# Kernel tuning notes

Measured on AMD Instinct MI355X. Metric: run time of the kernel, lower is better.

The kernel has to match this reference:

```python
import jax, jax.numpy as jnp
import numpy as np

# --- Clifford algebra constants for a 4D Euclidean space (MULTIVECTOR_DIM = 16) ---
# grades 0..4 have dims (1,4,6,4,1); component index -> grade:
GRADE_OF = np.array([0] + [1]*4 + [2]*6 + [3]*4 + [4], dtype=np.int64)  # [16]
# reversion sign per grade k: (-1)^{k(k-1)/2}
_REV_PER_GRADE = np.array([1.0, 1.0, -1.0, -1.0, 1.0], dtype=np.float32)
REVERSION = jnp.asarray(_REV_PER_GRADE[GRADE_OF])            # [16]
# scalar part of geometric product of orthonormal basis blades: diag of reversion signs
SCALAR_TABLE = jnp.asarray(np.diag(_REV_PER_GRADE[GRADE_OF]).astype(np.float32))  # [16,16]
SCALE = 1.0 / np.sqrt(16.0)

B, S, H, M = 4, 2048, 8, 16


def _block_masks():
    block = (GRADE_OF[:, None] == GRADE_OF[None, :]).astype(np.float32)  # [16,16]
    bias = ((GRADE_OF == 0) | (GRADE_OF == 4)).astype(np.float32)        # [16]
    return jnp.asarray(block), jnp.asarray(bias)


def setup_inputs() -> dict:
    key = jax.random.key(0)
    ks = jax.random.split(key, 10)
    block, bias = _block_masks()
    def w_in(k):   # [16, H, 16], zero outside grade blocks (j -> i within same grade)
        return jax.random.normal(k, (M, H, M), jnp.float32) * 0.1 * block[:, None, :]
    def b_in(k):   # [H, 16], only grade-0 / grade-4 components have bias
        return jax.random.normal(k, (H, M), jnp.float32) * 0.1 * bias[None, :]
    x = jax.random.normal(ks[0], (B, S, M), jnp.float32)
    return {
        "x": x,
        "wq": w_in(ks[1]), "bq": b_in(ks[2]),
        "wk": w_in(ks[3]), "bk": b_in(ks[4]),
        "wv": w_in(ks[5]), "bv": b_in(ks[6]),
        "wo": jax.random.normal(ks[7], (H, M, M), jnp.float32) * 0.1 * block[None, :, :],
        "bo": jax.random.normal(ks[8], (M,), jnp.float32) * 0.1 * bias,
    }


def reference(x, wq, bq, wk, bk, wv, bv, wo, bo):
    # per-grade Q/K/V projections, packed as block-sparse linears over 16 components
    q = jnp.einsum('bsj,jhi->bhsi', x, wq) + bq[None, :, None, :]  # [B,H,S,16]
    k = jnp.einsum('bsj,jhi->bhsi', x, wk) + bk[None, :, None, :]
    v = jnp.einsum('bsj,jhi->bhsi', x, wv) + bv[None, :, None, :]
    k_rev = k * REVERSION[None, None, None, :]
    # scalar part of geometric product <Q * reverse(K)>_0 via fixed bilinear table
    scores = jnp.einsum('bhqi,bhkj,ij->bhqk', q, k_rev, SCALAR_TABLE) * SCALE
    attn = jax.nn.softmax(scores, axis=-1)                         # [B,H,S,S]
    head = jnp.einsum('bhqk,bhki->bhqi', attn, v)                  # [B,H,S,16]
    # per-grade output projections (block over heads x grade components)
    out = jnp.einsum('bhqj,hji->bqi', head, wo) + bo               # [B,S,16]
    return out
```

## Files before the change

### kernel.cpp

```cpp
#include <hip/hip_runtime.h>

#define BB 4
#define SS 2048
#define HH 8
#define MM 16

#define QSCALE 0.36067376022224085f

typedef __attribute__((ext_vector_type(8)))  short short8;
typedef __attribute__((ext_vector_type(4)))  int   int4v;
typedef __attribute__((ext_vector_type(4)))  float f32x4;
typedef __attribute__((ext_vector_type(16))) float f32x16;

static constexpr size_t NQKV = (size_t)BB * HH * SS * MM;

__device__ __forceinline__ int pk_bf16(float lo, float hi) {
    int r;
    asm("v_cvt_pk_bf16_f32 %0, %1, %2" : "=v"(r) : "v"(lo), "v"(hi));
    return r;
}

__device__ __forceinline__ void proj16(const float xr[16], const float* __restrict__ w,
                                       const float* __restrict__ bias, int h, float out[16]) {
#pragma unroll
    for (int i = 0; i < 16; i++) out[i] = bias[(h << 4) + i];
#pragma unroll
    for (int j = 0; j < 16; j++) {
        float xj = xr[j];
        const float* wr = w + (((j * HH) + h) << 4);
#pragma unroll
        for (int i = 0; i < 16; i++) out[i] = fmaf(xj, wr[i], out[i]);
    }
}

__device__ __forceinline__ void pack_store(ushort* dst, const float o[16], float scale) {
    int4v w0, w1;
#pragma unroll
    for (int j = 0; j < 4; j++) w0[j] = pk_bf16(o[2*j] * scale,     o[2*j+1] * scale);
#pragma unroll
    for (int j = 0; j < 4; j++) w1[j] = pk_bf16(o[8+2*j] * scale,   o[8+2*j+1] * scale);
    int4v* p = (int4v*)dst;
    p[0] = w0; p[1] = w1;
}

__global__ __launch_bounds__(256) void proj_kernel(
    const float* __restrict__ x,
    const float* __restrict__ wq, const float* __restrict__ bq,
    const float* __restrict__ wk, const float* __restrict__ bk,
    const float* __restrict__ wv, const float* __restrict__ bv,
    ushort* __restrict__ qb, ushort* __restrict__ kb, ushort* __restrict__ vb)
{
    int h  = blockIdx.x >> 5;
    int bs = ((blockIdx.x & 31) << 8) + threadIdx.x;
    int b  = bs >> 11;

    float xr[16];
    const float4* x4 = (const float4*)(x + (size_t)bs * MM);
#pragma unroll
    for (int j = 0; j < 4; j++) {
        float4 t = x4[j];
        xr[j*4+0] = t.x; xr[j*4+1] = t.y; xr[j*4+2] = t.z; xr[j*4+3] = t.w;
    }

    size_t orow = (((size_t)(b * HH + h) * SS) + (bs & 2047)) * MM;
    float o[16];

    proj16(xr, wq, bq, h, o);  pack_store(qb + orow, o, QSCALE);
    proj16(xr, wk, bk, h, o);  pack_store(kb + orow, o, 1.0f);
    proj16(xr, wv, bv, h, o);  pack_store(vb + orow, o, 1.0f);
}

__global__ __launch_bounds__(256, 8) void attn_kernel(
    const ushort* __restrict__ qb, const ushort* __restrict__ kb,
    const ushort* __restrict__ vb, float* __restrict__ hb)
{
    __shared__ ushort Vl[4][32 * 72];

    int tid = threadIdx.x;
    int w = tid >> 6;
    int lane = tid & 63;
    int n = lane & 31, c = lane >> 5;

    int nb = ((blockIdx.x & 7) << 8) | (blockIdx.x >> 3);
    int bh = nb >> 6, qt = nb & 63;
    size_t base = (size_t)bh * SS * MM;
    const ushort* Qg = qb + base;
    const ushort* Kg = kb + base;
    const ushort* Vg = vb + base;

    int q = qt * 32 + n;
    short8 qf = *(const short8*)(Qg + (size_t)q * MM + c * 8);

    ushort* Vt = Vl[w];
    for (int i = lane; i < 72; i += 64) {
        Vt[16 * 72 + i] = 0x3F80;
        Vt[20 * 72 + i] = 0x3F80;
    }

    f32x16 oacc = 0;
    const f32x16 zacc = 0;

    int k0 = w * 512;
    int4v vwa = *(const int4v*)(Vg + (size_t)(k0 + lane) * MM);
    int4v vwb = *(const int4v*)(Vg + (size_t)(k0 + lane) * MM + 8);

    for (int t = 0; t < 8; t++) {
        union { int4v v; ushort s[8]; } ua, ub;
        ua.v = vwa; ub.v = vwb;
#pragma unroll
        for (int j = 0; j < 8; j++) Vt[j * 72 + lane] = ua.s[j];
#pragma unroll
        for (int j = 0; j < 8; j++) Vt[(8 + j) * 72 + lane] = ub.s[j];
        if (t != 7) {
            vwa = *(const int4v*)(Vg + (size_t)(k0 + (t + 1) * 64 + lane) * MM);
            vwb = *(const int4v*)(Vg + (size_t)(k0 + (t + 1) * 64 + lane) * MM + 8);
        }

#pragma unroll
        for (int sub = 0; sub < 2; sub++) {
            short8 kf = *(const short8*)(Kg + (size_t)(k0 + t * 64 + sub * 32 + n) * MM + c * 8);
            f32x16 s = __builtin_amdgcn_mfma_f32_32x32x16_bf16(kf, qf, zacc, 0, 0, 0);

            float pv[16];
#pragma unroll
            for (int r = 0; r < 16; r++) pv[r] = __builtin_amdgcn_exp2f(s[r]);

            int a0 = pk_bf16(pv[0],  pv[1]);
            int a1 = pk_bf16(pv[2],  pv[3]);
            int a2 = pk_bf16(pv[4],  pv[5]);
            int a3 = pk_bf16(pv[6],  pv[7]);
            int a4 = pk_bf16(pv[8],  pv[9]);
            int a5 = pk_bf16(pv[10], pv[11]);
            int a6 = pk_bf16(pv[12], pv[13]);
            int a7 = pk_bf16(pv[14], pv[15]);

            int w0 = a0, w2 = a2;
            asm("v_permlane32_swap_b32 %0, %1" : "+v"(w0), "+v"(w2));
            int w1 = a1, w3 = a3;
            asm("v_permlane32_swap_b32 %0, %1" : "+v"(w1), "+v"(w3));
            int u0 = a4, u2 = a6;
            asm("v_permlane32_swap_b32 %0, %1" : "+v"(u0), "+v"(u2));
            int u1 = a5, u3 = a7;
            asm("v_permlane32_swap_b32 %0, %1" : "+v"(u1), "+v"(u3));

            int4v bi1 = {w0, w1, w2, w3};
            int4v bi2 = {u0, u1, u2, u3};
            short8 B1 = __builtin_bit_cast(short8, bi1);
            short8 B2 = __builtin_bit_cast(short8, bi2);

            int vr = lane & 31;
            short8 vf1 = *(const short8*)&Vt[vr * 72 + sub * 32 + c * 8];
            short8 vf2 = *(const short8*)&Vt[vr * 72 + sub * 32 + 16 + c * 8];
            oacc = __builtin_amdgcn_mfma_f32_32x32x16_bf16(vf1, B1, oacc, 0, 0, 0);
            oacc = __builtin_amdgcn_mfma_f32_32x32x16_bf16(vf2, B2, oacc, 0, 0, 0);
        }
    }

    __syncthreads();
    float* mg = (float*)&Vl[0][0];
    if (w != 0) {
        float* dst = mg + (size_t)(w - 1) * 576 + n * 18;
#pragma unroll
        for (int j = 0; j < 4; j++) dst[4 * c + j]     = oacc[j];
#pragma unroll
        for (int j = 0; j < 4; j++) dst[8 + 4 * c + j] = oacc[4 + j];
        dst[16 + c] = oacc[8];
    }
    __syncthreads();
    if (w == 0) {
        float l = oacc[8];
        float o0[4], o1[4];
#pragma unroll
        for (int j = 0; j < 4; j++) { o0[j] = oacc[j]; o1[j] = oacc[4 + j]; }
#pragma unroll
        for (int p = 0; p < 3; p++) {
            const float* src = mg + (size_t)p * 576 + n * 18;
#pragma unroll
            for (int j = 0; j < 4; j++) o0[j] += src[4 * c + j];
#pragma unroll
            for (int j = 0; j < 4; j++) o1[j] += src[8 + 4 * c + j];
            l += src[16 + c];
        }
        float inv = 1.0f / l;
        float* orow = hb + base + (size_t)q * MM;
        f32x4 v0 = {o0[0] * inv, o0[1] * inv, o0[2] * inv, o0[3] * inv};
        f32x4 v1 = {o1[0] * inv, o1[1] * inv, o1[2] * inv, o1[3] * inv};
        *(f32x4*)(orow + 4 * c) = v0;
        *(f32x4*)(orow + 8 + 4 * c) = v1;
    }
}

__global__ __launch_bounds__(128) void outproj_kernel(
    const float* __restrict__ hb, const float* __restrict__ wo,
    const float* __restrict__ bo, float* __restrict__ out)
{
    int tid = threadIdx.x;
    int row = blockIdx.x * 64 + (tid >> 1);
    int hh = tid & 1;
    int b = row >> 11, s = row & 2047;

    float acc[16];
#pragma unroll
    for (int i = 0; i < 16; i++) acc[i] = 0.0f;

    for (int hi = 0; hi < 4; hi++) {
        int h = hh * 4 + hi;
        const float* hr = hb + ((size_t)(b * 8 + h) * SS + s) * MM;
        float hv[16];
        const f32x4* h4 = (const f32x4*)hr;
#pragma unroll
        for (int j = 0; j < 4; j++) {
            f32x4 tv = h4[j];
            hv[j*4+0] = tv[0]; hv[j*4+1] = tv[1]; hv[j*4+2] = tv[2]; hv[j*4+3] = tv[3];
        }
#pragma unroll
        for (int j = 0; j < 16; j++) {
            float hj = hv[j];
            const float* wr = wo + (((h << 4) + j) << 4);
#pragma unroll
            for (int i = 0; i < 16; i++) acc[i] = fmaf(hj, wr[i], acc[i]);
        }
    }

#pragma unroll
    for (int i = 0; i < 16; i++) acc[i] += __shfl_xor(acc[i], 1);

    if (hh == 0) {
        float* op = out + (size_t)row * MM;
#pragma unroll
        for (int j = 0; j < 4; j++) {
            f32x4 v = {acc[4*j+0] + bo[4*j+0], acc[4*j+1] + bo[4*j+1],
                       acc[4*j+2] + bo[4*j+2], acc[4*j+3] + bo[4*j+3]};
            *(f32x4*)(op + 4*j) = v;
        }
    }
}

extern "C" void kernel_launch(void* const* d_in, const int* in_sizes, int n_in,
                              void* d_out, int out_size, void* d_ws, size_t ws_size,
                              hipStream_t stream) {
    const float* x  = (const float*)d_in[0];
    const float* wq = (const float*)d_in[1];
    const float* bq = (const float*)d_in[2];
    const float* wk = (const float*)d_in[3];
    const float* bk = (const float*)d_in[4];
    const float* wv = (const float*)d_in[5];
    const float* bv = (const float*)d_in[6];
    const float* wo = (const float*)d_in[7];
    const float* bo = (const float*)d_in[8];
    float* out = (float*)d_out;

    ushort* qb = (ushort*)d_ws;
    ushort* kb = qb + NQKV;
    ushort* vb = kb + NQKV;
    float*  hb = (float*)(vb + NQKV);

    proj_kernel<<<256, 256, 0, stream>>>(x, wq, bq, wk, bk, wv, bv, qb, kb, vb);
    attn_kernel<<<2048, 256, 0, stream>>>(qb, kb, vb, hb);
    outproj_kernel<<<128, 128, 0, stream>>>(hb, wo, bo, out);
}
```

Measured before the change: 44.68 us.

## Store V transposed in global, drop LDS staging, add exp-minus-one precision split

The projection kernel now writes V transposed (dimension-major, sequence contiguous). This lets the attention kernel load V fragments straight from global memory instead of staging them through per-wave LDS, which removes the LDS writes and reads. The attention probabilities are packed as exp2(s)-1 in bf16 to keep more precision. The missing constant part is restored with extra MFMAs against a ones operand, so the PV MFMA count doubles. The unroll structure and launch bounds also change, and the V store in the projection becomes scattered 2-byte writes.

```diff
diff --git a/kernel.cpp b/kernel.cpp
--- a/kernel.cpp
+++ b/kernel.cpp
@@ -48,11 +48,13 @@
     const float* __restrict__ wq, const float* __restrict__ bq,
     const float* __restrict__ wk, const float* __restrict__ bk,
     const float* __restrict__ wv, const float* __restrict__ bv,
-    ushort* __restrict__ qb, ushort* __restrict__ kb, ushort* __restrict__ vb)
+    ushort* __restrict__ qb, ushort* __restrict__ kb, ushort* __restrict__ vt)
 {
     int h  = blockIdx.x >> 5;
     int bs = ((blockIdx.x & 31) << 8) + threadIdx.x;
     int b  = bs >> 11;
+    int s  = bs & 2047;
+    int bh = b * HH + h;
 
     float xr[16];
     const float4* x4 = (const float4*)(x + (size_t)bs * MM);
@@ -62,19 +64,25 @@
         xr[j*4+0] = t.x; xr[j*4+1] = t.y; xr[j*4+2] = t.z; xr[j*4+3] = t.w;
     }
 
-    size_t orow = (((size_t)(b * HH + h) * SS) + (bs & 2047)) * MM;
+    size_t orow = ((size_t)bh * SS + s) * MM;
     float o[16];
 
     proj16(xr, wq, bq, h, o);  pack_store(qb + orow, o, QSCALE);
     proj16(xr, wk, bk, h, o);  pack_store(kb + orow, o, 1.0f);
-    proj16(xr, wv, bv, h, o);  pack_store(vb + orow, o, 1.0f);
-}
-
-__global__ __launch_bounds__(256, 8) void attn_kernel(
+
+    proj16(xr, wv, bv, h, o);
+    ushort* vrow = vt + (size_t)bh * 16 * SS + s;
+#pragma unroll
+    for (int d = 0; d < 16; d++) {
+        vrow[(size_t)d * SS] = (ushort)pk_bf16(o[d], o[d]);
+    }
+}
+
+__global__ __launch_bounds__(256) void attn_kernel(
     const ushort* __restrict__ qb, const ushort* __restrict__ kb,
-    const ushort* __restrict__ vb, float* __restrict__ hb)
+    const ushort* __restrict__ vt, float* __restrict__ hb)
 {
-    __shared__ ushort Vl[4][32 * 72];
+    __shared__ float mg[3 * 32 * 18];
 
     int tid = threadIdx.x;
     int w = tid >> 6;
@@ -86,78 +94,70 @@
     size_t base = (size_t)bh * SS * MM;
     const ushort* Qg = qb + base;
     const ushort* Kg = kb + base;
-    const ushort* Vg = vb + base;
+    const ushort* Vtg = vt + (size_t)bh * 16 * SS;
 
     int q = qt * 32 + n;
     short8 qf = *(const short8*)(Qg + (size_t)q * MM + c * 8);
 
-    ushort* Vt = Vl[w];
-    for (int i = lane; i < 72; i += 64) {
-        Vt[16 * 72 + i] = 0x3F80;
-        Vt[20 * 72 + i] = 0x3F80;
-    }
+    short8 vfill = 0;
+    if (n == 16 || n == 20) {
+#pragma unroll
+        for (int j = 0; j < 8; j++) vfill[j] = (short)0x3F80;
+    }
+    short8 onesb;
+#pragma unroll
+    for (int j = 0; j < 8; j++) onesb[j] = (short)0x3F80;
 
     f32x16 oacc = 0;
     const f32x16 zacc = 0;
 
     int k0 = w * 512;
-    int4v vwa = *(const int4v*)(Vg + (size_t)(k0 + lane) * MM);
-    int4v vwb = *(const int4v*)(Vg + (size_t)(k0 + lane) * MM + 8);
-
-    for (int t = 0; t < 8; t++) {
-        union { int4v v; ushort s[8]; } ua, ub;
-        ua.v = vwa; ub.v = vwb;
-#pragma unroll
-        for (int j = 0; j < 8; j++) Vt[j * 72 + lane] = ua.s[j];
-#pragma unroll
-        for (int j = 0; j < 8; j++) Vt[(8 + j) * 72 + lane] = ub.s[j];
-        if (t != 7) {
-            vwa = *(const int4v*)(Vg + (size_t)(k0 + (t + 1) * 64 + lane) * MM);
-            vwb = *(const int4v*)(Vg + (size_t)(k0 + (t + 1) * 64 + lane) * MM + 8);
-        }
-
-#pragma unroll
-        for (int sub = 0; sub < 2; sub++) {
-            short8 kf = *(const short8*)(Kg + (size_t)(k0 + t * 64 + sub * 32 + n) * MM + c * 8);
-            f32x16 s = __builtin_amdgcn_mfma_f32_32x32x16_bf16(kf, qf, zacc, 0, 0, 0);
-
-            float pv[16];
-#pragma unroll
-            for (int r = 0; r < 16; r++) pv[r] = __builtin_amdgcn_exp2f(s[r]);
-
-            int a0 = pk_bf16(pv[0],  pv[1]);
-            int a1 = pk_bf16(pv[2],  pv[3]);
-            int a2 = pk_bf16(pv[4],  pv[5]);
-            int a3 = pk_bf16(pv[6],  pv[7]);
-            int a4 = pk_bf16(pv[8],  pv[9]);
-            int a5 = pk_bf16(pv[10], pv[11]);
-            int a6 = pk_bf16(pv[12], pv[13]);
-            int a7 = pk_bf16(pv[14], pv[15]);
-
-            int w0 = a0, w2 = a2;
-            asm("v_permlane32_swap_b32 %0, %1" : "+v"(w0), "+v"(w2));
-            int w1 = a1, w3 = a3;
-            asm("v_permlane32_swap_b32 %0, %1" : "+v"(w1), "+v"(w3));
-            int u0 = a4, u2 = a6;
-            asm("v_permlane32_swap_b32 %0, %1" : "+v"(u0), "+v"(u2));
-            int u1 = a5, u3 = a7;
-            asm("v_permlane32_swap_b32 %0, %1" : "+v"(u1), "+v"(u3));
-
-            int4v bi1 = {w0, w1, w2, w3};
-            int4v bi2 = {u0, u1, u2, u3};
-            short8 B1 = __builtin_bit_cast(short8, bi1);
-            short8 B2 = __builtin_bit_cast(short8, bi2);
-
-            int vr = lane & 31;
-            short8 vf1 = *(const short8*)&Vt[vr * 72 + sub * 32 + c * 8];
-            short8 vf2 = *(const short8*)&Vt[vr * 72 + sub * 32 + 16 + c * 8];
-            oacc = __builtin_amdgcn_mfma_f32_32x32x16_bf16(vf1, B1, oacc, 0, 0, 0);
-            oacc = __builtin_amdgcn_mfma_f32_32x32x16_bf16(vf2, B2, oacc, 0, 0, 0);
-        }
-    }
-
-    __syncthreads();
-    float* mg = (float*)&Vl[0][0];
+    const ushort* Kp  = Kg + (size_t)(k0 + n) * MM + c * 8;
+    const ushort* Vp  = Vtg + (size_t)n * SS + k0 + c * 8;
+
+#pragma unroll 2
+    for (int sub = 0; sub < 16; sub++) {
+        short8 kf = *(const short8*)(Kp + sub * 32 * MM);
+        f32x16 s = __builtin_amdgcn_mfma_f32_32x32x16_bf16(kf, qf, zacc, 0, 0, 0);
+
+        float pv[16];
+#pragma unroll
+        for (int r = 0; r < 16; r++) pv[r] = __builtin_amdgcn_exp2f(s[r]);
+#pragma unroll
+        for (int r = 0; r < 16; r++) pv[r] = pv[r] - 1.0f;
+
+        int a0 = pk_bf16(pv[0],  pv[1]);
+        int a1 = pk_bf16(pv[2],  pv[3]);
+        int a2 = pk_bf16(pv[4],  pv[5]);
+        int a3 = pk_bf16(pv[6],  pv[7]);
+        int a4 = pk_bf16(pv[8],  pv[9]);
+        int a5 = pk_bf16(pv[10], pv[11]);
+        int a6 = pk_bf16(pv[12], pv[13]);
+        int a7 = pk_bf16(pv[14], pv[15]);
+
+        int w0 = a0, w2 = a2;
+        asm("v_permlane32_swap_b32 %0, %1" : "+v"(w0), "+v"(w2));
+        int w1 = a1, w3 = a3;
+        asm("v_permlane32_swap_b32 %0, %1" : "+v"(w1), "+v"(w3));
+        int u0 = a4, u2 = a6;
+        asm("v_permlane32_swap_b32 %0, %1" : "+v"(u0), "+v"(u2));
+        int u1 = a5, u3 = a7;
+        asm("v_permlane32_swap_b32 %0, %1" : "+v"(u1), "+v"(u3));
+
+        int4v bi1 = {w0, w1, w2, w3};
+        int4v bi2 = {u0, u1, u2, u3};
+        short8 B1 = __builtin_bit_cast(short8, bi1);
+        short8 B2 = __builtin_bit_cast(short8, bi2);
+
+        const ushort* vsub = Vp + sub * 32;
+        short8 vf1 = (n < 16) ? *(const short8*)(vsub)      : vfill;
+        short8 vf2 = (n < 16) ? *(const short8*)(vsub + 16) : vfill;
+        oacc = __builtin_amdgcn_mfma_f32_32x32x16_bf16(vf1, onesb, oacc, 0, 0, 0);
+        oacc = __builtin_amdgcn_mfma_f32_32x32x16_bf16(vf1, B1,    oacc, 0, 0, 0);
+        oacc = __builtin_amdgcn_mfma_f32_32x32x16_bf16(vf2, onesb, oacc, 0, 0, 0);
+        oacc = __builtin_amdgcn_mfma_f32_32x32x16_bf16(vf2, B2,    oacc, 0, 0, 0);
+    }
+
     if (w != 0) {
         float* dst = mg + (size_t)(w - 1) * 576 + n * 18;
 #pragma unroll
@@ -252,10 +252,10 @@
 
     ushort* qb = (ushort*)d_ws;
     ushort* kb = qb + NQKV;
-    ushort* vb = kb + NQKV;
-    float*  hb = (float*)(vb + NQKV);
-
-    proj_kernel<<<256, 256, 0, stream>>>(x, wq, bq, wk, bk, wv, bv, qb, kb, vb);
-    attn_kernel<<<2048, 256, 0, stream>>>(qb, kb, vb, hb);
+    ushort* vt = kb + NQKV;
+    float*  hb = (float*)(vt + NQKV);
+
+    proj_kernel<<<256, 256, 0, stream>>>(x, wq, bq, wk, bk, wv, bv, qb, kb, vt);
+    attn_kernel<<<2048, 256, 0, stream>>>(qb, kb, vt, hb);
     outproj_kernel<<<128, 128, 0, stream>>>(hb, wo, bo, out);
 }
```

Measured after the change: 55.22 us. +23.6%, slower.

## Share staged K/V tiles across two query waves and center exp to improve bf16 precision

Applied to the files above, without the earlier changes.

Blocks now hold 512 threads, and each 128-thread group serves 64 queries with two waves that share K and V tiles staged in LDS. K now comes from shared memory instead of per-wave global loads, which halves global K/V traffic per query. Probabilities are computed as exp2(s)-1 before bf16 packing, and the missing term is restored with column sums of V and a constant 2048 added to the normalizer. This adds two block barriers per tile and a per-tile column-sum pass.

```diff
diff --git a/kernel.cpp b/kernel.cpp
--- a/kernel.cpp
+++ b/kernel.cpp
@@ -70,117 +70,170 @@
     proj16(xr, wv, bv, h, o);  pack_store(vb + orow, o, 1.0f);
 }
 
-__global__ __launch_bounds__(256, 8) void attn_kernel(
+__global__ __launch_bounds__(512) void attn_kernel(
     const ushort* __restrict__ qb, const ushort* __restrict__ kb,
     const ushort* __restrict__ vb, float* __restrict__ hb)
 {
-    __shared__ ushort Vl[4][32 * 72];
+    __shared__ ushort stage[4][3840];
 
     int tid = threadIdx.x;
-    int w = tid >> 6;
+    int grp = tid >> 7, t7 = tid & 127;
+    int wid2 = (tid >> 6) & 1;
     int lane = tid & 63;
     int n = lane & 31, c = lane >> 5;
 
-    int nb = ((blockIdx.x & 7) << 8) | (blockIdx.x >> 3);
-    int bh = nb >> 6, qt = nb & 63;
+    int nb = ((blockIdx.x & 7) << 7) | (blockIdx.x >> 3);
+    int bh = nb >> 5, qt = nb & 31;
     size_t base = (size_t)bh * SS * MM;
     const ushort* Qg = qb + base;
     const ushort* Kg = kb + base;
     const ushort* Vg = vb + base;
 
-    int q = qt * 32 + n;
+    int q = qt * 64 + wid2 * 32 + n;
     short8 qf = *(const short8*)(Qg + (size_t)q * MM + c * 8);
 
-    ushort* Vt = Vl[w];
-    for (int i = lane; i < 72; i += 64) {
+    ushort* Kl = &stage[grp][0];
+    ushort* Vt = &stage[grp][1536];
+
+    for (int i = t7; i < 72; i += 128) {
         Vt[16 * 72 + i] = 0x3F80;
         Vt[20 * 72 + i] = 0x3F80;
-    }
+#pragma unroll
+        for (int r = 17; r < 20; r++) Vt[r * 72 + i] = 0;
+#pragma unroll
+        for (int r = 21; r < 32; r++) Vt[r * 72 + i] = 0;
+    }
+
+    int k0 = grp * 512;
+    int srow = t7 >> 1, shalf = t7 & 1;
+
+    {
+        int4v kw = *(const int4v*)(Kg + (size_t)(k0 + srow) * MM + shalf * 8);
+        int4v vw = *(const int4v*)(Vg + (size_t)(k0 + srow) * MM + shalf * 8);
+        *(int4v*)&Kl[srow * 24 + shalf * 8] = kw;
+        union { int4v v; ushort s[8]; } vu; vu.v = vw;
+#pragma unroll
+        for (int j = 0; j < 8; j++) Vt[(8 * shalf + j) * 72 + srow] = vu.s[j];
+    }
+    __syncthreads();
 
     f32x16 oacc = 0;
     const f32x16 zacc = 0;
-
-    int k0 = w * 512;
-    int4v vwa = *(const int4v*)(Vg + (size_t)(k0 + lane) * MM);
-    int4v vwb = *(const int4v*)(Vg + (size_t)(k0 + lane) * MM + 8);
+    float cs = 0.0f;
+    int csd = lane >> 2, cspart = lane & 3;
 
     for (int t = 0; t < 8; t++) {
-        union { int4v v; ushort s[8]; } ua, ub;
-        ua.v = vwa; ub.v = vwb;
-#pragma unroll
-        for (int j = 0; j < 8; j++) Vt[j * 72 + lane] = ua.s[j];
-#pragma unroll
-        for (int j = 0; j < 8; j++) Vt[(8 + j) * 72 + lane] = ub.s[j];
+        int4v kw2, vw2;
         if (t != 7) {
-            vwa = *(const int4v*)(Vg + (size_t)(k0 + (t + 1) * 64 + lane) * MM);
-            vwb = *(const int4v*)(Vg + (size_t)(k0 + (t + 1) * 64 + lane) * MM + 8);
+            kw2 = *(const int4v*)(Kg + (size_t)(k0 + (t + 1) * 64 + srow) * MM + shalf * 8);
+            vw2 = *(const int4v*)(Vg + (size_t)(k0 + (t + 1) * 64 + srow) * MM + shalf * 8);
         }
 
 #pragma unroll
         for (int sub = 0; sub < 2; sub++) {
-            short8 kf = *(const short8*)(Kg + (size_t)(k0 + t * 64 + sub * 32 + n) * MM + c * 8);
+            short8 kf = *(const short8*)&Kl[(sub * 32 + n) * 24 + c * 8];
+            short8 vf1 = *(const short8*)&Vt[n * 72 + sub * 32 + c * 8];
+            short8 vf2 = *(const short8*)&Vt[n * 72 + sub * 32 + 16 + c * 8];
             f32x16 s = __builtin_amdgcn_mfma_f32_32x32x16_bf16(kf, qf, zacc, 0, 0, 0);
 
-            float pv[16];
-#pragma unroll
-            for (int r = 0; r < 16; r++) pv[r] = __builtin_amdgcn_exp2f(s[r]);
-
-            int a0 = pk_bf16(pv[0],  pv[1]);
-            int a1 = pk_bf16(pv[2],  pv[3]);
-            int a2 = pk_bf16(pv[4],  pv[5]);
-            int a3 = pk_bf16(pv[6],  pv[7]);
-            int a4 = pk_bf16(pv[8],  pv[9]);
-            int a5 = pk_bf16(pv[10], pv[11]);
-            int a6 = pk_bf16(pv[12], pv[13]);
-            int a7 = pk_bf16(pv[14], pv[15]);
-
+            float p0 = __builtin_amdgcn_exp2f(s[0])  - 1.0f;
+            float p1 = __builtin_amdgcn_exp2f(s[1])  - 1.0f;
+            float p2 = __builtin_amdgcn_exp2f(s[2])  - 1.0f;
+            float p3 = __builtin_amdgcn_exp2f(s[3])  - 1.0f;
+            float p4 = __builtin_amdgcn_exp2f(s[4])  - 1.0f;
+            float p5 = __builtin_amdgcn_exp2f(s[5])  - 1.0f;
+            float p6 = __builtin_amdgcn_exp2f(s[6])  - 1.0f;
+            float p7 = __builtin_amdgcn_exp2f(s[7])  - 1.0f;
+            int a0 = pk_bf16(p0, p1), a1 = pk_bf16(p2, p3);
+            int a2 = pk_bf16(p4, p5), a3 = pk_bf16(p6, p7);
             int w0 = a0, w2 = a2;
             asm("v_permlane32_swap_b32 %0, %1" : "+v"(w0), "+v"(w2));
             int w1 = a1, w3 = a3;
             asm("v_permlane32_swap_b32 %0, %1" : "+v"(w1), "+v"(w3));
+            int4v bi1 = {w0, w1, w2, w3};
+            short8 B1 = __builtin_bit_cast(short8, bi1);
+            oacc = __builtin_amdgcn_mfma_f32_32x32x16_bf16(vf1, B1, oacc, 0, 0, 0);
+
+            float p8  = __builtin_amdgcn_exp2f(s[8])  - 1.0f;
+            float p9  = __builtin_amdgcn_exp2f(s[9])  - 1.0f;
+            float p10 = __builtin_amdgcn_exp2f(s[10]) - 1.0f;
+            float p11 = __builtin_amdgcn_exp2f(s[11]) - 1.0f;
+            float p12 = __builtin_amdgcn_exp2f(s[12]) - 1.0f;
+            float p13 = __builtin_amdgcn_exp2f(s[13]) - 1.0f;
+            float p14 = __builtin_amdgcn_exp2f(s[14]) - 1.0f;
+            float p15 = __builtin_amdgcn_exp2f(s[15]) - 1.0f;
+            int a4 = pk_bf16(p8,  p9),  a5 = pk_bf16(p10, p11);
+            int a6 = pk_bf16(p12, p13), a7 = pk_bf16(p14, p15);
             int u0 = a4, u2 = a6;
             asm("v_permlane32_swap_b32 %0, %1" : "+v"(u0), "+v"(u2));
             int u1 = a5, u3 = a7;
             asm("v_permlane32_swap_b32 %0, %1" : "+v"(u1), "+v"(u3));
-
-            int4v bi1 = {w0, w1, w2, w3};
             int4v bi2 = {u0, u1, u2, u3};
-            short8 B1 = __builtin_bit_cast(short8, bi1);
             short8 B2 = __builtin_bit_cast(short8, bi2);
-
-            int vr = lane & 31;
-            short8 vf1 = *(const short8*)&Vt[vr * 72 + sub * 32 + c * 8];
-            short8 vf2 = *(const short8*)&Vt[vr * 72 + sub * 32 + 16 + c * 8];
-            oacc = __builtin_amdgcn_mfma_f32_32x32x16_bf16(vf1, B1, oacc, 0, 0, 0);
             oacc = __builtin_amdgcn_mfma_f32_32x32x16_bf16(vf2, B2, oacc, 0, 0, 0);
         }
-    }
-
-    __syncthreads();
-    float* mg = (float*)&Vl[0][0];
-    if (w != 0) {
-        float* dst = mg + (size_t)(w - 1) * 576 + n * 18;
+
+        {
+            int4v u0 = *(const int4v*)&Vt[csd * 72 + cspart * 16];
+            int4v u1 = *(const int4v*)&Vt[csd * 72 + cspart * 16 + 8];
+#pragma unroll
+            for (int j = 0; j < 4; j++) {
+                cs += __builtin_bit_cast(float, u0[j] << 16);
+                cs += __builtin_bit_cast(float, (int)(u0[j] & 0xFFFF0000));
+                cs += __builtin_bit_cast(float, u1[j] << 16);
+                cs += __builtin_bit_cast(float, (int)(u1[j] & 0xFFFF0000));
+            }
+        }
+
+        __syncthreads();
+        if (t != 7) {
+            *(int4v*)&Kl[srow * 24 + shalf * 8] = kw2;
+            union { int4v v; ushort s[8]; } vu; vu.v = vw2;
+#pragma unroll
+            for (int j = 0; j < 8; j++) Vt[(8 * shalf + j) * 72 + srow] = vu.s[j];
+        }
+        __syncthreads();
+    }
+
+    cs += __shfl_xor(cs, 1);
+    cs += __shfl_xor(cs, 2);
+
+    float* mgf = (float*)&stage[0][0];
+    int ql = wid2 * 32 + n;
+    if (grp != 0) {
+        float* dst = mgf + (size_t)(grp - 1) * 1152 + ql * 18;
 #pragma unroll
         for (int j = 0; j < 4; j++) dst[4 * c + j]     = oacc[j];
 #pragma unroll
         for (int j = 0; j < 4; j++) dst[8 + 4 * c + j] = oacc[4 + j];
         dst[16 + c] = oacc[8];
     }
+    if (wid2 == 0 && cspart == 0) mgf[3456 + grp * 16 + csd] = cs;
     __syncthreads();
-    if (w == 0) {
+
+    if (grp == 0) {
         float l = oacc[8];
         float o0[4], o1[4];
 #pragma unroll
         for (int j = 0; j < 4; j++) { o0[j] = oacc[j]; o1[j] = oacc[4 + j]; }
 #pragma unroll
         for (int p = 0; p < 3; p++) {
-            const float* src = mg + (size_t)p * 576 + n * 18;
+            const float* src = mgf + (size_t)p * 1152 + ql * 18;
 #pragma unroll
             for (int j = 0; j < 4; j++) o0[j] += src[4 * c + j];
 #pragma unroll
             for (int j = 0; j < 4; j++) o1[j] += src[8 + 4 * c + j];
             l += src[16 + c];
         }
+#pragma unroll
+        for (int w = 0; w < 4; w++) {
+#pragma unroll
+            for (int j = 0; j < 4; j++) o0[j] += mgf[3456 + w * 16 + 4 * c + j];
+#pragma unroll
+            for (int j = 0; j < 4; j++) o1[j] += mgf[3456 + w * 16 + 8 + 4 * c + j];
+        }
+        l += 2048.0f;
+
         float inv = 1.0f / l;
         float* orow = hb + base + (size_t)q * MM;
         f32x4 v0 = {o0[0] * inv, o0[1] * inv, o0[2] * inv, o0[3] * inv};
@@ -256,6 +309,6 @@
     float*  hb = (float*)(vb + NQKV);
 
     proj_kernel<<<256, 256, 0, stream>>>(x, wq, bq, wk, bk, wv, bv, qb, kb, vb);
-    attn_kernel<<<2048, 256, 0, stream>>>(qb, kb, vb, hb);
+    attn_kernel<<<1024, 512, 0, stream>>>(qb, kb, vb, hb);
     outproj_kernel<<<128, 128, 0, stream>>>(hb, wo, bo, out);
 }
```

Measured after the change: 52.70 us. +17.9%, slower.
